# Kernel optimization log

Hardware: AMD Instinct MI355X
Metric: run time of the kernel (lower is better)

The kernel has to match this reference:

```python
import jax, jax.numpy as jnp
import numpy as np

SIGMA = 0.3
EPS = 1e-8  # torch CosineSimilarity eps
LOG_SQRT_2PI = float(0.5 * np.log(2.0 * np.pi))


def setup_inputs() -> dict:
    key = jax.random.key(0)
    k1, k2 = jax.random.split(key)
    Ex = jax.random.normal(k1, (8192, 256), dtype=jnp.float32)
    Ey = jax.random.normal(k2, (8192, 256), dtype=jnp.float32)
    return {"Ex": Ex, "Ey": Ey}


def reference(Ex, Ey):
    # cosine similarity: normalize rows (clamped norms), then dot -> [n, m]
    xn = Ex / jnp.maximum(jnp.linalg.norm(Ex, axis=-1, keepdims=True), EPS)
    yn = Ey / jnp.maximum(jnp.linalg.norm(Ey, axis=-1, keepdims=True), EPS)
    M = jnp.einsum('nd,md->nm', xn, yn)
    # Normal(loc=1, scale=sigma).log_prob
    z = (M - 1.0) / SIGMA
    logp = -0.5 * z * z - jnp.log(jnp.asarray(SIGMA, M.dtype)) - LOG_SQRT_2PI
    # C = -(exp(logp) * logp); row-wise min over y-tokens -> [n]
    C = -jnp.exp(logp) * logp
    return jnp.min(C, axis=-1)
```

## Files before the change

### kernel.cpp

```cpp
#include <hip/hip_runtime.h>
#include <hip/hip_bf16.h>

typedef unsigned short u16;
typedef __attribute__((ext_vector_type(8))) short short8;
typedef __attribute__((ext_vector_type(4))) float floatx4;

#define NROWS 8192
#define DIM 256
#define BM 128
#define BNT 128
#define NCT 4
#define NKB 8
#define BK 32

__device__ __forceinline__ void atomicMinFloat(float* addr, float val) {
    if (val >= 0.0f) {
        atomicMin((int*)addr, __float_as_int(val));
    } else {
        atomicMax((unsigned int*)addr, __float_as_uint(val));
    }
}

__device__ __forceinline__ u16 f32_to_bf16_rne(float x) {
    unsigned int u = __float_as_uint(x);
    unsigned int r = (u + 0x7fffu + ((u >> 16) & 1u)) >> 16;
    return (u16)r;
}

__device__ __forceinline__ float c_of_m(float m) {
    const float INV_SIG = 1.0f / 0.3f;
    const float KC = 0.28503427f;
    float z = (m - 1.0f) * INV_SIG;
    float logp = fmaf(-0.5f * z, z, KC);
    return -logp * __expf(logp);
}

__device__ __forceinline__ void load16(const u16* g, u16* l) {
    __builtin_amdgcn_global_load_lds(
        (__attribute__((address_space(1))) void*)g,
        (__attribute__((address_space(3))) void*)l, 16, 0, 0);
}

__global__ __launch_bounds__(256) void normalize_kernel(const float* __restrict__ Ex,
                                                        const float* __restrict__ Ey,
                                                        u16* __restrict__ Xn,
                                                        u16* __restrict__ Yn,
                                                        float* __restrict__ out) {
    const int t = threadIdx.x;
    const int lane = t & 63;
    const int row = blockIdx.x * 4 + (t >> 6);
    const float* src = (blockIdx.y == 0) ? Ex : Ey;
    u16* dst = (blockIdx.y == 0) ? Xn : Yn;

    float4 v = *(const float4*)(src + (size_t)row * DIM + lane * 4);
    float s = fmaf(v.x, v.x, fmaf(v.y, v.y, fmaf(v.z, v.z, v.w * v.w)));
    #pragma unroll
    for (int m = 32; m >= 1; m >>= 1) s += __shfl_xor(s, m, 64);
    float inv = 1.0f / fmaxf(sqrtf(s), 1e-8f);

    ushort4 o;
    o.x = f32_to_bf16_rne(v.x * inv);
    o.y = f32_to_bf16_rne(v.y * inv);
    o.z = f32_to_bf16_rne(v.z * inv);
    o.w = f32_to_bf16_rne(v.w * inv);
    *(ushort4*)(dst + (size_t)row * DIM + lane * 4) = o;

    if (blockIdx.y == 0 && lane == 0) out[row] = __uint_as_float(0x7f800000u);
}

__global__ __launch_bounds__(256, 2) void gemm_min_kernel(const u16* __restrict__ Xn,
                                                          const u16* __restrict__ Yn,
                                                          float* __restrict__ out) {
    __shared__ u16 As[NKB][BM * BK];
    __shared__ u16 Bs[2][BNT * BK];

    const int tid = threadIdx.x;
    const int w = tid >> 6;
    const int lane = tid & 63;
    const int wr = w >> 1;
    const int wc = w & 1;
    const int lq = lane >> 4;
    const int lm = lane & 15;
    const int swz = (lm >> 1) & 3;

    const int b = blockIdx.x;
    const int rowStart = (b & 63) * BM;
    const int colBase = (b >> 6) * (NCT * BNT);

    const int s0 = w * 64 + lane;
    const int s1 = s0 + 256;
    const int r0 = s0 >> 2, p0 = (s0 & 3) ^ ((r0 >> 1) & 3);
    const int r1 = s1 >> 2, p1 = (s1 & 3) ^ ((r1 >> 1) & 3);
    const int go0 = r0 * DIM + p0 * 8;
    const int go1 = r1 * DIM + p1 * 8;
    const int lo0 = (w * 64) * 8;
    const int lo1 = (256 + w * 64) * 8;

    {
        const u16* xb = Xn + (size_t)rowStart * DIM;
        #pragma unroll
        for (int kb = 0; kb < NKB; ++kb) {
            load16(xb + go0 + kb * BK, &As[kb][lo0]);
            load16(xb + go1 + kb * BK, &As[kb][lo1]);
        }
        const u16* yb = Yn + (size_t)colBase * DIM;
        load16(yb + go0, &Bs[0][lo0]);
        load16(yb + go1, &Bs[0][lo1]);
    }

    int aoff[4], boff[4];
    #pragma unroll
    for (int rg = 0; rg < 4; ++rg)
        aoff[rg] = ((wr * 64 + rg * 16 + lm) * 4 + (lq ^ swz)) * 8;
    #pragma unroll
    for (int cg = 0; cg < 4; ++cg)
        boff[cg] = ((wc * 64 + cg * 16 + lm) * 4 + (lq ^ swz)) * 8;

    floatx4 mn4[4], mx4[4];
    #pragma unroll
    for (int rg = 0; rg < 4; ++rg) {
        mn4[rg] = (floatx4){3.4e38f, 3.4e38f, 3.4e38f, 3.4e38f};
        mx4[rg] = (floatx4){-3.4e38f, -3.4e38f, -3.4e38f, -3.4e38f};
    }

    for (int ct = 0; ct < NCT; ++ct) {
        floatx4 acc[4][4];
        #pragma unroll
        for (int i = 0; i < 4; ++i)
            #pragma unroll
            for (int j = 0; j < 4; ++j)
                acc[i][j] = (floatx4){0.0f, 0.0f, 0.0f, 0.0f};

        #pragma unroll
        for (int kt = 0; kt < NKB; ++kt) {
            __syncthreads();
            if (!(ct == NCT - 1 && kt == NKB - 1)) {
                int nct = ct, nkt = kt + 1;
                if (nkt == NKB) { nkt = 0; nct = ct + 1; }
                const u16* yb = Yn + (size_t)(colBase + nct * BNT) * DIM + nkt * BK;
                load16(yb + go0, &Bs[nkt & 1][lo0]);
                load16(yb + go1, &Bs[nkt & 1][lo1]);
            }

            const int buf = kt & 1;
            short8 a[4], bb[4];
            #pragma unroll
            for (int rg = 0; rg < 4; ++rg)
                a[rg] = *(const short8*)(&As[kt][aoff[rg]]);
            #pragma unroll
            for (int cg = 0; cg < 4; ++cg)
                bb[cg] = *(const short8*)(&Bs[buf][boff[cg]]);

            #pragma unroll
            for (int rg = 0; rg < 4; ++rg)
                #pragma unroll
                for (int cg = 0; cg < 4; ++cg)
                    acc[rg][cg] = __builtin_amdgcn_mfma_f32_16x16x32_bf16(a[rg], bb[cg], acc[rg][cg], 0, 0, 0);
        }

        #pragma unroll
        for (int rg = 0; rg < 4; ++rg)
            #pragma unroll
            for (int cg = 0; cg < 4; ++cg)
                #pragma unroll
                for (int r = 0; r < 4; ++r) {
                    float m = acc[rg][cg][r];
                    mn4[rg][r] = fminf(mn4[rg][r], m);
                    mx4[rg][r] = fmaxf(mx4[rg][r], m);
                }
    }

    #pragma unroll
    for (int rg = 0; rg < 4; ++rg) {
        #pragma unroll
        for (int r = 0; r < 4; ++r) {
            float mn = mn4[rg][r];
            float mx = mx4[rg][r];
            #pragma unroll
            for (int mofs = 1; mofs < 16; mofs <<= 1) {
                mn = fminf(mn, __shfl_xor(mn, mofs, 64));
                mx = fmaxf(mx, __shfl_xor(mx, mofs, 64));
            }
            if (lm == 0) {
                float cmin = fminf(c_of_m(mn), c_of_m(mx));
                int row = rowStart + wr * 64 + rg * 16 + lq * 4 + r;
                atomicMinFloat(&out[row], cmin);
            }
        }
    }
}

extern "C" void kernel_launch(void* const* d_in, const int* in_sizes, int n_in,
                              void* d_out, int out_size, void* d_ws, size_t ws_size,
                              hipStream_t stream) {
    const float* Ex = (const float*)d_in[0];
    const float* Ey = (const float*)d_in[1];
    float* out = (float*)d_out;
    u16* Xn = (u16*)d_ws;
    u16* Yn = Xn + (size_t)NROWS * DIM;

    hipLaunchKernelGGL(normalize_kernel, dim3(NROWS / 4, 2), dim3(256), 0, stream,
                       Ex, Ey, Xn, Yn, out);
    hipLaunchKernelGGL(gemm_min_kernel, dim3(64 * (NROWS / (NCT * BNT))), dim3(256), 0, stream,
                       Xn, Yn, out);
}
```

Baseline: 109.0 us.

## Pre-pack Y into MFMA fragment layout and stream B operands directly into registers

The normalize kernel now writes normalized Ey in a panel layout that matches the MFMA B-fragment order, one 16-row panel per k-step and lane. The GEMM drops the shared-memory B double buffer and the per-k-step __syncthreads. Each wave instead loads its B fragments straight from global memory into registers, with a one-step register prefetch. This removes LDS traffic and barrier stalls for B. In exchange, B is fetched twice per block (once per row-wave pair) through L2/global, and global latency may be exposed with only one step of prefetch.

```diff
diff --git a/kernel.cpp b/kernel.cpp
--- a/kernel.cpp
+++ b/kernel.cpp
@@ -44,15 +44,14 @@
 __global__ __launch_bounds__(256) void normalize_kernel(const float* __restrict__ Ex,
                                                         const float* __restrict__ Ey,
                                                         u16* __restrict__ Xn,
-                                                        u16* __restrict__ Yn,
+                                                        u16* __restrict__ Ys,
                                                         float* __restrict__ out) {
     const int t = threadIdx.x;
-    const int lane = t & 63;
+    const int ln = t & 63;
     const int row = blockIdx.x * 4 + (t >> 6);
     const float* src = (blockIdx.y == 0) ? Ex : Ey;
-    u16* dst = (blockIdx.y == 0) ? Xn : Yn;
-
-    float4 v = *(const float4*)(src + (size_t)row * DIM + lane * 4);
+
+    float4 v = *(const float4*)(src + (size_t)row * DIM + ln * 4);
     float s = fmaf(v.x, v.x, fmaf(v.y, v.y, fmaf(v.z, v.z, v.w * v.w)));
     #pragma unroll
     for (int m = 32; m >= 1; m >>= 1) s += __shfl_xor(s, m, 64);
@@ -63,16 +62,25 @@
     o.y = f32_to_bf16_rne(v.y * inv);
     o.z = f32_to_bf16_rne(v.z * inv);
     o.w = f32_to_bf16_rne(v.w * inv);
-    *(ushort4*)(dst + (size_t)row * DIM + lane * 4) = o;
-
-    if (blockIdx.y == 0 && lane == 0) out[row] = __uint_as_float(0x7f800000u);
+
+    if (blockIdx.y == 0) {
+        *(ushort4*)(Xn + (size_t)row * DIM + ln * 4) = o;
+        if (ln == 0) out[row] = __uint_as_float(0x7f800000u);
+    } else {
+        const int p = row >> 4;
+        const int lm = row & 15;
+        const int kt = ln >> 3;
+        const int lq = (ln >> 1) & 3;
+        const int j4 = (ln & 1) * 4;
+        const size_t off = ((size_t)((p * NKB + kt) * 64 + lq * 16 + lm)) * 8 + j4;
+        *(ushort4*)(Ys + off) = o;
+    }
 }
 
 __global__ __launch_bounds__(256, 2) void gemm_min_kernel(const u16* __restrict__ Xn,
-                                                          const u16* __restrict__ Yn,
+                                                          const u16* __restrict__ Ys,
                                                           float* __restrict__ out) {
     __shared__ u16 As[NKB][BM * BK];
-    __shared__ u16 Bs[2][BNT * BK];
 
     const int tid = threadIdx.x;
     const int w = tid >> 6;
@@ -85,36 +93,34 @@
 
     const int b = blockIdx.x;
     const int rowStart = (b & 63) * BM;
-    const int colBase = (b >> 6) * (NCT * BNT);
-
-    const int s0 = w * 64 + lane;
-    const int s1 = s0 + 256;
-    const int r0 = s0 >> 2, p0 = (s0 & 3) ^ ((r0 >> 1) & 3);
-    const int r1 = s1 >> 2, p1 = (s1 & 3) ^ ((r1 >> 1) & 3);
-    const int go0 = r0 * DIM + p0 * 8;
-    const int go1 = r1 * DIM + p1 * 8;
-    const int lo0 = (w * 64) * 8;
-    const int lo1 = (256 + w * 64) * 8;
+    const int colPanBase = (b >> 6) * 32 + wc * 4;
 
     {
+        const int s0 = w * 64 + lane;
+        const int s1 = s0 + 256;
+        const int r0 = s0 >> 2, p0 = (s0 & 3) ^ ((r0 >> 1) & 3);
+        const int r1 = s1 >> 2, p1 = (s1 & 3) ^ ((r1 >> 1) & 3);
+        const int go0 = r0 * DIM + p0 * 8;
+        const int go1 = r1 * DIM + p1 * 8;
+        const int lo0 = (w * 64) * 8;
+        const int lo1 = (256 + w * 64) * 8;
         const u16* xb = Xn + (size_t)rowStart * DIM;
         #pragma unroll
         for (int kb = 0; kb < NKB; ++kb) {
             load16(xb + go0 + kb * BK, &As[kb][lo0]);
             load16(xb + go1 + kb * BK, &As[kb][lo1]);
         }
-        const u16* yb = Yn + (size_t)colBase * DIM;
-        load16(yb + go0, &Bs[0][lo0]);
-        load16(yb + go1, &Bs[0][lo1]);
-    }
-
-    int aoff[4], boff[4];
+    }
+
+    int aoff[4];
     #pragma unroll
     for (int rg = 0; rg < 4; ++rg)
         aoff[rg] = ((wr * 64 + rg * 16 + lm) * 4 + (lq ^ swz)) * 8;
+
+    const u16* bp[4];
     #pragma unroll
     for (int cg = 0; cg < 4; ++cg)
-        boff[cg] = ((wc * 64 + cg * 16 + lm) * 4 + (lq ^ swz)) * 8;
+        bp[cg] = Ys + (size_t)(colPanBase + cg) * (NKB * 64 * 8) + lane * 8;
 
     floatx4 mn4[4], mx4[4];
     #pragma unroll
@@ -123,6 +129,14 @@
         mx4[rg] = (floatx4){-3.4e38f, -3.4e38f, -3.4e38f, -3.4e38f};
     }
 
+    __syncthreads();
+
+    short8 bbuf[2][4];
+    #pragma unroll
+    for (int cg = 0; cg < 4; ++cg)
+        bbuf[0][cg] = *(const short8*)(bp[cg]);
+
+    #pragma unroll
     for (int ct = 0; ct < NCT; ++ct) {
         floatx4 acc[4][4];
         #pragma unroll
@@ -133,29 +147,28 @@
 
         #pragma unroll
         for (int kt = 0; kt < NKB; ++kt) {
-            __syncthreads();
-            if (!(ct == NCT - 1 && kt == NKB - 1)) {
-                int nct = ct, nkt = kt + 1;
-                if (nkt == NKB) { nkt = 0; nct = ct + 1; }
-                const u16* yb = Yn + (size_t)(colBase + nct * BNT) * DIM + nkt * BK;
-                load16(yb + go0, &Bs[nkt & 1][lo0]);
-                load16(yb + go1, &Bs[nkt & 1][lo1]);
-            }
-
-            const int buf = kt & 1;
-            short8 a[4], bb[4];
+            short8 a[4];
             #pragma unroll
             for (int rg = 0; rg < 4; ++rg)
                 a[rg] = *(const short8*)(&As[kt][aoff[rg]]);
-            #pragma unroll
-            for (int cg = 0; cg < 4; ++cg)
-                bb[cg] = *(const short8*)(&Bs[buf][boff[cg]]);
+
+            if (kt < NKB - 1) {
+                #pragma unroll
+                for (int cg = 0; cg < 4; ++cg)
+                    bbuf[(kt + 1) & 1][cg] =
+                        *(const short8*)(bp[cg] + (ct * (NKB * 8) + (kt + 1)) * 512 / 8 * 8);
+            } else if (ct < NCT - 1) {
+                #pragma unroll
+                for (int cg = 0; cg < 4; ++cg)
+                    bbuf[0][cg] = *(const short8*)(bp[cg] + ((ct + 1) * (NKB * 8)) * 512);
+            }
 
             #pragma unroll
             for (int rg = 0; rg < 4; ++rg)
                 #pragma unroll
                 for (int cg = 0; cg < 4; ++cg)
-                    acc[rg][cg] = __builtin_amdgcn_mfma_f32_16x16x32_bf16(a[rg], bb[cg], acc[rg][cg], 0, 0, 0);
+                    acc[rg][cg] = __builtin_amdgcn_mfma_f32_16x16x32_bf16(
+                        a[rg], bbuf[kt & 1][cg], acc[rg][cg], 0, 0, 0);
         }
 
         #pragma unroll
@@ -197,10 +210,10 @@
     const float* Ey = (const float*)d_in[1];
     float* out = (float*)d_out;
     u16* Xn = (u16*)d_ws;
-    u16* Yn = Xn + (size_t)NROWS * DIM;
+    u16* Ys = Xn + (size_t)NROWS * DIM;
 
     hipLaunchKernelGGL(normalize_kernel, dim3(NROWS / 4, 2), dim3(256), 0, stream,
-                       Ex, Ey, Xn, Yn, out);
+                       Ex, Ey, Xn, Ys, out);
     hipLaunchKernelGGL(gemm_min_kernel, dim3(64 * (NROWS / (NCT * BNT))), dim3(256), 0, stream,
-                       Xn, Yn, out);
-}
+                       Xn, Ys, out);
+}
```

Result: slower. 288.3 us (+164.5%).
